# Optimization experiments

Measured on AMD Instinct MI355X. Metric: run time of the kernel, lower is better.

## Reference

```python
import jax, jax.numpy as jnp
import numpy as np

B, T, C = 2, 2048, 1024
N_HEAD = 16
G_NON = 32   # qgroup_size_non (layernorm / residual path)
G_LIN = 32   # qgroup_size_lin (linear path)
QMAX = 127.0
EPS = 1e-5


def quantize(x, G):
    """Group-wise symmetric int8 quantization along the last dim.
    Returns q (int8, same shape as x) and scales s with shape x.shape[:-1] + (D//G,)."""
    shp = x.shape
    xg = x.reshape(shp[:-1] + (shp[-1] // G, G))
    s = jnp.maximum(jnp.max(jnp.abs(xg), axis=-1) / QMAX, 1e-8)
    q = jnp.clip(jnp.round(xg / s[..., None]), -QMAX, QMAX).astype(jnp.int8)
    return q.reshape(shp), s


def dequant(q, s, G):
    shp = q.shape
    xg = q.astype(jnp.float32).reshape(shp[:-1] + (shp[-1] // G, G)) * s[..., None]
    return xg.reshape(shp)


def quant_dequant(x, G):
    """Fake-quantize (straight-through): forward = dequant(quantize(x))."""
    q, s = quantize(x, G)
    xd = dequant(q, s, G)
    return x + jax.lax.stop_gradient(xd - x)


def setup_inputs() -> dict:
    key = jax.random.key(0)
    k1, k2, k3, k4 = jax.random.split(key, 4)
    x = jax.random.normal(k1, (B, T, C), dtype=jnp.float32)
    # LN stats of x, produced by the previous block's int8_add_..._MeanVar
    mean = jnp.mean(x, axis=-1)
    rstd = 1.0 / jnp.sqrt(jnp.var(x, axis=-1) + EPS)
    qx, sx = quantize(x, G_NON)
    ln_w = 1.0 + 0.02 * jax.random.normal(k2, (C,), dtype=jnp.float32)
    w1 = 0.02 * jax.random.normal(k3, (3 * C, C), dtype=jnp.float32)   # c_attn.weight [out,in]
    w2 = 0.02 * jax.random.normal(k4, (C, C), dtype=jnp.float32)       # c_proj.weight [out,in]
    return {"x": x, "qx": qx.astype(jnp.int32), "sx": sx, "mean": mean,
            "rstd": rstd, "ln_w": ln_w, "w1": w1, "w2": w2}


def reference(x, qx, sx, mean, rstd, ln_w, w1, w2):
    hd = C // N_HEAD
    # ---- Part1: int8 layernorm (uses provided mean/rstd) + int8 c_attn linear ----
    ln_in = dequant(qx.astype(jnp.int8), sx, G_NON)               # [B,T,C]
    h = (ln_in - mean[..., None]) * rstd[..., None] * ln_w        # layernorm output
    hq = quant_dequant(h, G_NON)                                  # requantize activations
    w1q = quant_dequant(w1, G_LIN)                                # int8 weight
    qkv = jnp.einsum('btc,oc->bto', hq, w1q)                      # [B,T,3C]
    q, k, v = jnp.split(qkv, 3, axis=-1)
    q = q.reshape(B, T, N_HEAD, hd).transpose(0, 2, 1, 3)         # [B,H,T,hd]
    k = k.reshape(B, T, N_HEAD, hd).transpose(0, 2, 1, 3)
    v = v.reshape(B, T, N_HEAD, hd).transpose(0, 2, 1, 3)
    # ---- causal SDPA ----
    scores = jnp.einsum('bhqd,bhkd->bhqk', q, k) / jnp.sqrt(jnp.float32(hd))
    causal = jnp.tril(jnp.ones((T, T), dtype=bool))
    scores = jnp.where(causal, scores, jnp.float32(-1e30))
    attn = jax.nn.softmax(scores, axis=-1)
    y = jnp.einsum('bhqk,bhkd->bhqd', attn, v)
    y = y.transpose(0, 2, 1, 3).reshape(B, T, C)
    # ---- Part2: int8 c_proj linear + residual add with mean/var ----
    yq = quant_dequant(y, G_LIN)
    w2q = quant_dequant(w2, G_LIN)
    proj = jnp.einsum('btc,oc->bto', yq, w2q)
    fpx = x + proj                                                # fp residual output
    mean_o = jnp.mean(fpx, axis=-1)
    rstd_o = 1.0 / jnp.sqrt(jnp.var(fpx, axis=-1) + EPS)
    qo, so = quantize(fpx, G_NON)                                 # quantized output for next block
    return (fpx, qo, so, mean_o, rstd_o)
```

## Files before the change

### kernel.cpp

```cpp
#include <hip/hip_runtime.h>
#include <stdint.h>

#define BB 2
#define TT 2048
#define CC 1024
#define NH 16
#define HD 64
#define NG 32
#define ROWS (BB*TT)
#define C3 (3*CC)

typedef _Float16 half_t;
typedef __attribute__((ext_vector_type(8))) _Float16 half8;
typedef __attribute__((ext_vector_type(2))) __fp16 fp16x2;
typedef __attribute__((ext_vector_type(4))) float f32x4;

#define GLDS16(g, l) __builtin_amdgcn_global_load_lds( \
    (__attribute__((address_space(1))) void*)(g), \
    (__attribute__((address_space(3))) void*)(l), 16, 0, 0)

#define LOG2E 1.44269504f
#define DEFER_THR 5.5451774f

__device__ __forceinline__ uint32_t pk_h2(float a, float b) {
  union { fp16x2 h; uint32_t u; } cv;
  cv.h = __builtin_amdgcn_cvt_pkrtz(a, b);
  return cv.u;
}

__global__ void k_qdq_w(const float* __restrict__ w1, const float* __restrict__ w2,
                        half_t* __restrict__ o1, half_t* __restrict__ o2) {
  int g = blockIdx.x * blockDim.x + threadIdx.x;
  const float* src; half_t* dst; int gl;
  if (g < C3 * NG) { src = w1; dst = o1; gl = g; }
  else             { src = w2; dst = o2; gl = g - C3 * NG; }
  const float4* p = reinterpret_cast<const float4*>(src + (size_t)gl * 32);
  float v[32]; float amax = 0.f;
  #pragma unroll
  for (int i = 0; i < 8; ++i) {
    float4 t = p[i];
    v[4*i] = t.x; v[4*i+1] = t.y; v[4*i+2] = t.z; v[4*i+3] = t.w;
    amax = fmaxf(amax, fmaxf(fmaxf(fabsf(t.x), fabsf(t.y)), fmaxf(fabsf(t.z), fabsf(t.w))));
  }
  float s = fmaxf(amax / 127.0f, 1e-8f);
  half_t* o = dst + (size_t)gl * 32;
  #pragma unroll
  for (int c = 0; c < 4; ++c) {
    half8 ov;
    #pragma unroll
    for (int jj = 0; jj < 8; ++jj) {
      float q = fminf(fmaxf(rintf(v[c*8+jj] / s), -127.f), 127.f);
      ov[jj] = (half_t)(q * s);
    }
    *reinterpret_cast<half8*>(o + c*8) = ov;
  }
}

__global__ void k_qh(const int* __restrict__ qx, const float* __restrict__ sx,
                     const float* __restrict__ mean, const float* __restrict__ rstd,
                     const float* __restrict__ lnw, half_t* __restrict__ h16) {
  int g = blockIdx.x * blockDim.x + threadIdx.x;
  if (g >= ROWS * NG) return;
  int row = g >> 5, grp = g & 31;
  float sxv = sx[g];
  float mu = mean[row], rs = rstd[row];
  const int4* qp = reinterpret_cast<const int4*>(qx + (size_t)row * CC + grp * 32);
  const float4* wp = reinterpret_cast<const float4*>(lnw + grp * 32);
  float v[32]; float amax = 0.f;
  #pragma unroll
  for (int i = 0; i < 8; ++i) {
    int4 qv = qp[i]; float4 wv = wp[i];
    float h0 = ((float)qv.x * sxv - mu) * rs * wv.x;
    float h1 = ((float)qv.y * sxv - mu) * rs * wv.y;
    float h2 = ((float)qv.z * sxv - mu) * rs * wv.z;
    float h3 = ((float)qv.w * sxv - mu) * rs * wv.w;
    v[4*i] = h0; v[4*i+1] = h1; v[4*i+2] = h2; v[4*i+3] = h3;
    amax = fmaxf(amax, fmaxf(fmaxf(fabsf(h0), fabsf(h1)), fmaxf(fabsf(h2), fabsf(h3))));
  }
  float s = fmaxf(amax / 127.0f, 1e-8f);
  half_t* o = h16 + (size_t)row * CC + grp * 32;
  #pragma unroll
  for (int c = 0; c < 4; ++c) {
    half8 ov;
    #pragma unroll
    for (int jj = 0; jj < 8; ++jj) {
      float q = fminf(fmaxf(rintf(v[c*8+jj] / s), -127.f), 127.f);
      ov[jj] = (half_t)(q * s);
    }
    *reinterpret_cast<half8*>(o + c*8) = ov;
  }
}

template<typename TO>
__global__ __launch_bounds__(256) void k_gemm16(const half_t* __restrict__ A,
                                                const half_t* __restrict__ B,
                                                TO* __restrict__ Out, int N,
                                                int gx, int cpx, int klen) {
  __shared__ __align__(16) half_t As[2][128*32];
  __shared__ __align__(16) half_t Bs[2][128*32];
  const int tid = threadIdx.x;
  const int wave = tid >> 6, lane = tid & 63;
  const int l15 = lane & 15, lg = lane >> 4;
  const int flat = blockIdx.y * gx + blockIdx.x;
  const int swz = (flat & 7) * cpx + (flat >> 3);
  const int m0 = (swz / gx) * 128, n0 = (swz % gx) * 128;
  const int kbeg = blockIdx.z * klen;
  TO* out = Out + (size_t)blockIdx.z * ROWS * N;
  const int wm = (wave >> 1) * 64, wn = (wave & 1) * 64;
  f32x4 acc[4][4];
  #pragma unroll
  for (int i = 0; i < 4; ++i)
    #pragma unroll
    for (int jj = 0; jj < 4; ++jj) acc[i][jj] = f32x4{0.f, 0.f, 0.f, 0.f};
  const int srow = lane >> 2;
  const int scol = (lane & 3) * 8;
  const int seg0 = wave * 2;
  auto stage = [&](int buf, int k0) {
    #pragma unroll
    for (int s = 0; s < 2; ++s) {
      const int seg = seg0 + s;
      GLDS16(A + (size_t)(m0 + seg*16 + srow) * 1024 + k0 + scol, &As[buf][0] + seg*512);
      GLDS16(B + (size_t)(n0 + seg*16 + srow) * 1024 + k0 + scol, &Bs[buf][0] + seg*512);
    }
  };
  stage(0, kbeg);
  __syncthreads();
  int cur = 0;
  for (int k0 = kbeg; k0 < kbeg + klen; k0 += 32) {
    if (k0 + 32 < kbeg + klen) stage(cur ^ 1, k0 + 32);
    half8 af[4], bf[4];
    #pragma unroll
    for (int i = 0; i < 4; ++i) {
      af[i] = *reinterpret_cast<const half8*>(&As[cur][0] + (wm + i*16 + l15)*32 + lg*8);
      bf[i] = *reinterpret_cast<const half8*>(&Bs[cur][0] + (wn + i*16 + l15)*32 + lg*8);
    }
    #pragma unroll
    for (int mi = 0; mi < 4; ++mi)
      #pragma unroll
      for (int ni = 0; ni < 4; ++ni)
        acc[mi][ni] = __builtin_amdgcn_mfma_f32_16x16x32_f16(af[mi], bf[ni], acc[mi][ni], 0, 0, 0);
    __syncthreads();
    cur ^= 1;
  }
  const int crow = m0 + wm + lg * 4;
  const int ccol = n0 + wn + l15;
  #pragma unroll
  for (int mi = 0; mi < 4; ++mi)
    #pragma unroll
    for (int ni = 0; ni < 4; ++ni)
      #pragma unroll
      for (int r = 0; r < 4; ++r)
        out[(size_t)(crow + mi*16 + r) * N + ccol + ni*16] = (TO)acc[mi][ni][r];
}

__global__ __launch_bounds__(512, 4) void k_attn16(const half_t* __restrict__ qkv,
                                                   half_t* __restrict__ y16) {
  __shared__ __align__(16) half_t Ks[2][64*72];
  __shared__ __align__(16) half_t Vt[2][64*72];
  __shared__ __align__(16) half_t Ps[8][16*72];
  const int tid = threadIdx.x;
  const int wave = tid >> 6, lane = tid & 63;
  const int l15 = lane & 15, lg = lane >> 4;
  const int w4 = wave & 3;
  const int bh = blockIdx.x, b = bh >> 4, h = bh & 15;
  const int j = blockIdx.y;
  const int qtB = 31 - j;
  const int qt = (wave >> 2) ? qtB : j;

  const size_t row = (size_t)(b * TT + qt * 64 + w4 * 16 + l15);
  const half_t* qp = qkv + row * C3 + h * HD + lg * 8;
  const half8 q0 = *reinterpret_cast<const half8*>(qp)      * (half_t)0.125f;
  const half8 q1 = *reinterpret_cast<const half8*>(qp + 32) * (half_t)0.125f;

  float m = -3.0e38f;
  f32x4 yacc[4];
  f32x4 lacc = f32x4{0,0,0,0};
  #pragma unroll
  for (int n = 0; n < 4; ++n) yacc[n] = f32x4{0,0,0,0};

  const int sj = tid >> 3, sc = (tid & 7) * 8;
  const int vkp = tid >> 4, vd0 = (tid & 15) * 4;
  const int vxor = ((vd0 >> 3) & 7) << 2;
  const int pxor = (l15 & 3) << 3;
  half_t* pw = &Ps[wave][0];

  int vdw0[4], vdw1[4];
  #pragma unroll
  for (int n = 0; n < 4; ++n) {
    const int d = n*16 + l15;
    const int x = ((n*2 + (l15 >> 3)) & 7) << 2;
    vdw0[n] = (d*36 + lg*4) ^ x;
    vdw1[n] = (d*36 + 16 + lg*4) ^ x;
  }

  half8 ones8;
  #pragma unroll
  for (int i = 0; i < 8; ++i) ones8[i] = (half_t)1.0f;

  half8 k0r; uint2 u0r, u1r;
  const half_t* kvb = qkv + ((size_t)b * TT) * C3 + CC + h * HD;
  auto kload = [&](int kt) {
    const half_t* kp = kvb + (size_t)(kt*64 + sj) * C3 + sc;
    k0r = *reinterpret_cast<const half8*>(kp);
    const half_t* vp = kvb + (size_t)(kt*64 + vkp*2) * C3 + CC + vd0;
    u0r = *reinterpret_cast<const uint2*>(vp);
    u1r = *reinterpret_cast<const uint2*>(vp + C3);
  };
  auto stage = [&](int buf) {
    *reinterpret_cast<half8*>(&Ks[buf][0] + sj*72 + sc) = k0r;
    uint32_t* vt32 = reinterpret_cast<uint32_t*>(&Vt[buf][0]);
    vt32[((vd0+0)*36 + vkp) ^ vxor] = __builtin_amdgcn_perm(u1r.x, u0r.x, 0x05040100u);
    vt32[((vd0+1)*36 + vkp) ^ vxor] = __builtin_amdgcn_perm(u1r.x, u0r.x, 0x07060302u);
    vt32[((vd0+2)*36 + vkp) ^ vxor] = __builtin_amdgcn_perm(u1r.y, u0r.y, 0x05040100u);
    vt32[((vd0+3)*36 + vkp) ^ vxor] = __builtin_amdgcn_perm(u1r.y, u0r.y, 0x07060302u);
  };

  kload(0);
  stage(0);
  kload(1);
  __syncthreads();
  for (int kt = 0; kt <= qtB; ++kt) {
    const int cur = kt & 1;
    if (kt < qtB) {
      stage(cur ^ 1);
      if (kt + 2 <= qtB) kload(kt + 2);
    }
    if (kt <= qt) {
      const half_t* ksb = &Ks[cur][0];
      const uint32_t* vt32 = reinterpret_cast<const uint32_t*>(&Vt[cur][0]);
      f32x4 sacc[4];
      __builtin_amdgcn_s_setprio(1);
      #pragma unroll
      for (int kg = 0; kg < 4; ++kg) {
        const half8 a0 = *reinterpret_cast<const half8*>(ksb + (kg*16 + l15)*72 + lg*8);
        const half8 a1 = *reinterpret_cast<const half8*>(ksb + (kg*16 + l15)*72 + lg*8 + 32);
        f32x4 t = f32x4{0,0,0,0};
        t = __builtin_amdgcn_mfma_f32_16x16x32_f16(a0, q0, t, 0, 0, 0);
        t = __builtin_amdgcn_mfma_f32_16x16x32_f16(a1, q1, t, 0, 0, 0);
        sacc[kg] = t;
      }
      __builtin_amdgcn_s_setprio(0);
      float sv[16]; float tm = -3.0e38f;
      const bool diag = (kt == qt);
      #pragma unroll
      for (int kg = 0; kg < 4; ++kg)
        #pragma unroll
        for (int r = 0; r < 4; ++r) {
          float s = sacc[kg][r];
          if (diag && (kg*16 + lg*4 + r > w4*16 + l15)) s = -1e30f;
          sv[kg*4 + r] = s;
          tm = fmaxf(tm, s);
        }
      tm = fmaxf(tm, __shfl_xor(tm, 16));
      tm = fmaxf(tm, __shfl_xor(tm, 32));
      if (!__all(tm <= m + DEFER_THR)) {
        const float mn = fmaxf(m, tm);
        const float alpha = __builtin_amdgcn_exp2f((m - mn) * LOG2E);
        #pragma unroll
        for (int n = 0; n < 4; ++n) yacc[n] *= alpha;
        lacc *= alpha;
        m = mn;
      }
      const float nm = -m * LOG2E;
      #pragma unroll
      for (int i = 0; i < 16; ++i)
        sv[i] = __builtin_amdgcn_exp2f(fmaf(sv[i], LOG2E, nm));
      uint32_t* prow = reinterpret_cast<uint32_t*>(pw) + l15*36;
      #pragma unroll
      for (int kg = 0; kg < 4; ++kg) {
        uint2 pr;
        pr.x = pk_h2(sv[kg*4 + 0], sv[kg*4 + 1]);
        pr.y = pk_h2(sv[kg*4 + 2], sv[kg*4 + 3]);
        *reinterpret_cast<uint2*>(prow + ((kg*8 + lg*2) ^ pxor)) = pr;
      }
      __builtin_amdgcn_sched_barrier(0);
      const half8 pb0 = *reinterpret_cast<const half8*>(
          pw + (l15*36 + ((lg*4) ^ pxor)) * 2);
      const half8 pb1 = *reinterpret_cast<const half8*>(
          pw + (l15*36 + ((16 + lg*4) ^ pxor)) * 2);
      __builtin_amdgcn_s_setprio(1);
      #pragma unroll
      for (int n = 0; n < 4; ++n) {
        const half8 va0 = *reinterpret_cast<const half8*>(vt32 + vdw0[n]);
        const half8 va1 = *reinterpret_cast<const half8*>(vt32 + vdw1[n]);
        yacc[n] = __builtin_amdgcn_mfma_f32_16x16x32_f16(va0, pb0, yacc[n], 0, 0, 0);
        yacc[n] = __builtin_amdgcn_mfma_f32_16x16x32_f16(va1, pb1, yacc[n], 0, 0, 0);
      }
      lacc = __builtin_amdgcn_mfma_f32_16x16x32_f16(ones8, pb0, lacc, 0, 0, 0);
      lacc = __builtin_amdgcn_mfma_f32_16x16x32_f16(ones8, pb1, lacc, 0, 0, 0);
      __builtin_amdgcn_s_setprio(0);
    }
    __syncthreads();
  }

  const float inv = 1.0f / lacc[0];
  float v[16];
  #pragma unroll
  for (int n = 0; n < 4; ++n)
    #pragma unroll
    for (int r = 0; r < 4; ++r) v[n*4 + r] = yacc[n][r] * inv;
  half_t* yp = y16 + row * CC + h * HD;
  #pragma unroll
  for (int g = 0; g < 2; ++g) {
    float am = 0.f;
    #pragma unroll
    for (int t = 0; t < 8; ++t) am = fmaxf(am, fabsf(v[g*8 + t]));
    am = fmaxf(am, __shfl_xor(am, 16));
    am = fmaxf(am, __shfl_xor(am, 32));
    const float s = fmaxf(am / 127.0f, 1e-8f);
    const float qi = 1.0f / s;
    #pragma unroll
    for (int nn = 0; nn < 2; ++nn) {
      const int n = g*2 + nn;
      union { half_t h4[4]; uint64_t u; } pk;
      #pragma unroll
      for (int r = 0; r < 4; ++r) {
        float q = fminf(fmaxf(rintf(v[n*4 + r] * qi), -127.f), 127.f);
        pk.h4[r] = (half_t)(q * s);
      }
      *reinterpret_cast<uint64_t*>(yp + n*16 + lg*4) = pk.u;
    }
  }
}

__global__ __launch_bounds__(256) void k_final(
    const float* __restrict__ x, const half_t* __restrict__ p0,
    const half_t* __restrict__ p1,
    float* __restrict__ out_fpx, float* __restrict__ out_qo, float* __restrict__ out_so,
    float* __restrict__ out_mean, float* __restrict__ out_rstd) {
  __shared__ float red[16];
  int row = blockIdx.x;
  int tid = threadIdx.x;
  size_t base = (size_t)row * CC + tid * 4;
  float4 xv = *reinterpret_cast<const float4*>(x + base);
  union { uint64_t u; half_t h[4]; } pa, pb;
  pa.u = *reinterpret_cast<const uint64_t*>(p0 + base);
  pb.u = *reinterpret_cast<const uint64_t*>(p1 + base);
  float4 f;
  f.x = xv.x + (float)pa.h[0] + (float)pb.h[0];
  f.y = xv.y + (float)pa.h[1] + (float)pb.h[1];
  f.z = xv.z + (float)pa.h[2] + (float)pb.h[2];
  f.w = xv.w + (float)pa.h[3] + (float)pb.h[3];
  *reinterpret_cast<float4*>(out_fpx + base) = f;
  float sum = f.x + f.y + f.z + f.w;
  float sq  = f.x*f.x + f.y*f.y + f.z*f.z + f.w*f.w;
  #pragma unroll
  for (int off = 1; off < 64; off <<= 1) {
    sum += __shfl_xor(sum, off);
    sq  += __shfl_xor(sq, off);
  }
  int wid = tid >> 6, lane = tid & 63;
  if (lane == 0) { red[wid] = sum; red[8 + wid] = sq; }
  __syncthreads();
  if (tid == 0) {
    float s4 = red[0] + red[1] + red[2] + red[3];
    float q4 = red[8] + red[9] + red[10] + red[11];
    float mu = s4 * (1.0f / CC);
    float var = q4 * (1.0f / CC) - mu * mu;
    out_mean[row] = mu;
    out_rstd[row] = 1.0f / sqrtf(var + 1e-5f);
  }
  float amax = fmaxf(fmaxf(fabsf(f.x), fabsf(f.y)), fmaxf(fabsf(f.z), fabsf(f.w)));
  #pragma unroll
  for (int off = 1; off < 8; off <<= 1) amax = fmaxf(amax, __shfl_xor(amax, off, 8));
  float s = fmaxf(amax / 127.0f, 1e-8f);
  int g = tid >> 3, li = tid & 7;
  if (li == 0) out_so[row * NG + g] = s;
  float4 qo;
  qo.x = fminf(fmaxf(rintf(f.x / s), -127.f), 127.f);
  qo.y = fminf(fmaxf(rintf(f.y / s), -127.f), 127.f);
  qo.z = fminf(fmaxf(rintf(f.z / s), -127.f), 127.f);
  qo.w = fminf(fmaxf(rintf(f.w / s), -127.f), 127.f);
  *reinterpret_cast<float4*>(out_qo + base) = qo;
}

extern "C" void kernel_launch(void* const* d_in, const int* in_sizes, int n_in,
                              void* d_out, int out_size, void* d_ws, size_t ws_size,
                              hipStream_t stream) {
  const float* x    = (const float*)d_in[0];
  const int*   qx   = (const int*)d_in[1];
  const float* sx   = (const float*)d_in[2];
  const float* mean = (const float*)d_in[3];
  const float* rstd = (const float*)d_in[4];
  const float* lnw  = (const float*)d_in[5];
  const float* w1   = (const float*)d_in[6];
  const float* w2   = (const float*)d_in[7];

  float* out = (float*)d_out;
  float* o_fpx  = out;
  float* o_qo   = o_fpx + (size_t)ROWS * CC;
  float* o_so   = o_qo  + (size_t)ROWS * CC;
  float* o_mean = o_so  + (size_t)ROWS * NG;
  float* o_rstd = o_mean + ROWS;

  size_t off = 0;
  char* wsb = (char*)d_ws;
  auto alloc = [&](size_t bytes) -> void* {
    void* p = wsb + off;
    off += (bytes + 255) & ~(size_t)255;
    return p;
  };
  half_t* h16   = (half_t*)alloc((size_t)ROWS * CC * 2);
  half_t* w116  = (half_t*)alloc((size_t)C3 * CC * 2);
  half_t* w216  = (half_t*)alloc((size_t)CC * CC * 2);
  half_t* qkv16 = (half_t*)alloc((size_t)ROWS * C3 * 2);
  half_t* y16   = (half_t*)alloc((size_t)ROWS * CC * 2);
  half_t* proj  = (half_t*)alloc((size_t)2 * ROWS * CC * 2);

  k_qdq_w<<<(C3 * NG + CC * NG) / 256, 256, 0, stream>>>(w1, w2, w116, w216);
  k_qh<<<(ROWS * NG) / 256, 256, 0, stream>>>(qx, sx, mean, rstd, lnw, h16);
  k_gemm16<half_t><<<dim3(C3 / 128, ROWS / 128, 1), 256, 0, stream>>>(
      h16, w116, qkv16, C3, C3 / 128, (C3 / 128) * (ROWS / 128) / 8, 1024);
  k_attn16<<<dim3(BB * NH, 16), 512, 0, stream>>>(qkv16, y16);
  k_gemm16<half_t><<<dim3(CC / 128, ROWS / 128, 2), 256, 0, stream>>>(
      y16, w216, proj, CC, CC / 128, (CC / 128) * (ROWS / 128) / 8, 512);
  k_final<<<ROWS, 256, 0, stream>>>(x, proj, proj + (size_t)ROWS * CC,
                                    o_fpx, o_qo, o_so, o_mean, o_rstd);
}
```

Baseline: 125.9 us.

## Rewrite attention with 32x32 MFMA, register-resident P, and split-KV wave pairs

The attention kernel moves from 16x16x32 to 32x32x16 MFMA tiles. Each wave now owns 32 query rows, and the P tile stays in registers as the B operand, so the per-wave LDS round trip for P goes away. The row sum is taken directly instead of through a ones-vector MFMA. Wave pairs split the KV tiles by parity and merge their partial softmax states through shared memory at the end, with a permuted V column layout to match the new register mapping. The risks are higher register pressure from the 16-wide accumulators, an extra sync and merge step, and each wave doing work only every other KV tile.

```diff
diff --git a/kernel.cpp b/kernel.cpp
--- a/kernel.cpp
+++ b/kernel.cpp
@@ -14,6 +14,7 @@
 typedef __attribute__((ext_vector_type(8))) _Float16 half8;
 typedef __attribute__((ext_vector_type(2))) __fp16 fp16x2;
 typedef __attribute__((ext_vector_type(4))) float f32x4;
+typedef __attribute__((ext_vector_type(16))) float f32x16;
 
 #define GLDS16(g, l) __builtin_amdgcn_global_load_lds( \
     (__attribute__((address_space(1))) void*)(g), \
@@ -153,49 +154,41 @@
         out[(size_t)(crow + mi*16 + r) * N + ccol + ni*16] = (TO)acc[mi][ni][r];
 }
 
-__global__ __launch_bounds__(512, 4) void k_attn16(const half_t* __restrict__ qkv,
+__global__ __launch_bounds__(512, 4) void k_attn32(const half_t* __restrict__ qkv,
                                                    half_t* __restrict__ y16) {
-  __shared__ __align__(16) half_t Ks[2][64*72];
-  __shared__ __align__(16) half_t Vt[2][64*72];
-  __shared__ __align__(16) half_t Ps[8][16*72];
+  __shared__ __align__(16) half_t smem[4][64*72];
   const int tid = threadIdx.x;
   const int wave = tid >> 6, lane = tid & 63;
-  const int l15 = lane & 15, lg = lane >> 4;
-  const int w4 = wave & 3;
+  const int l31 = lane & 31, lh = lane >> 5;
   const int bh = blockIdx.x, b = bh >> 4, h = bh & 15;
   const int j = blockIdx.y;
-  const int qtB = 31 - j;
-  const int qt = (wave >> 2) ? qtB : j;
-
-  const size_t row = (size_t)(b * TT + qt * 64 + w4 * 16 + l15);
-  const half_t* qp = qkv + row * C3 + h * HD + lg * 8;
-  const half8 q0 = *reinterpret_cast<const half8*>(qp)      * (half_t)0.125f;
-  const half8 q1 = *reinterpret_cast<const half8*>(qp + 32) * (half_t)0.125f;
-
-  float m = -3.0e38f;
-  f32x4 yacc[4];
-  f32x4 lacc = f32x4{0,0,0,0};
-  #pragma unroll
-  for (int n = 0; n < 4; ++n) yacc[n] = f32x4{0,0,0,0};
+  const int tile = wave >> 2, par = (wave >> 1) & 1, rh = wave & 1;
+  const int qt = tile ? (31 - j) : j;
+  const int ktmax = 31 - j;
+
+  const size_t qrow = (size_t)(b * TT + qt * 64 + rh * 32 + l31);
+  const half_t* qp = qkv + qrow * C3 + h * HD + lh * 8;
+  half8 qreg[4];
+  #pragma unroll
+  for (int kk = 0; kk < 4; ++kk)
+    qreg[kk] = *reinterpret_cast<const half8*>(qp + kk * 16) * (half_t)0.125f;
+
+  float m = -3.0e38f, lsum = 0.f;
+  f32x16 yacc[2];
+  yacc[0] = (f32x16)(0.f); yacc[1] = (f32x16)(0.f);
 
   const int sj = tid >> 3, sc = (tid & 7) * 8;
   const int vkp = tid >> 4, vd0 = (tid & 15) * 4;
+  const int csp = (vkp & 0x19) | ((vkp & 2) << 1) | ((vkp & 4) >> 1);
   const int vxor = ((vd0 >> 3) & 7) << 2;
-  const int pxor = (l15 & 3) << 3;
-  half_t* pw = &Ps[wave][0];
-
-  int vdw0[4], vdw1[4];
-  #pragma unroll
-  for (int n = 0; n < 4; ++n) {
-    const int d = n*16 + l15;
-    const int x = ((n*2 + (l15 >> 3)) & 7) << 2;
-    vdw0[n] = (d*36 + lg*4) ^ x;
-    vdw1[n] = (d*36 + 16 + lg*4) ^ x;
-  }
-
-  half8 ones8;
-  #pragma unroll
-  for (int i = 0; i < 8; ++i) ones8[i] = (half_t)1.0f;
+
+  int vbase[2], vxr[2];
+  #pragma unroll
+  for (int db = 0; db < 2; ++db) {
+    const int d = db * 32 + l31;
+    vbase[db] = d * 36 + lh * 4;
+    vxr[db] = ((d >> 3) & 7) << 2;
+  }
 
   half8 k0r; uint2 u0r, u1r;
   const half_t* kvb = qkv + ((size_t)b * TT) * C3 + CC + h * HD;
@@ -207,118 +200,141 @@
     u1r = *reinterpret_cast<const uint2*>(vp + C3);
   };
   auto stage = [&](int buf) {
-    *reinterpret_cast<half8*>(&Ks[buf][0] + sj*72 + sc) = k0r;
-    uint32_t* vt32 = reinterpret_cast<uint32_t*>(&Vt[buf][0]);
-    vt32[((vd0+0)*36 + vkp) ^ vxor] = __builtin_amdgcn_perm(u1r.x, u0r.x, 0x05040100u);
-    vt32[((vd0+1)*36 + vkp) ^ vxor] = __builtin_amdgcn_perm(u1r.x, u0r.x, 0x07060302u);
-    vt32[((vd0+2)*36 + vkp) ^ vxor] = __builtin_amdgcn_perm(u1r.y, u0r.y, 0x05040100u);
-    vt32[((vd0+3)*36 + vkp) ^ vxor] = __builtin_amdgcn_perm(u1r.y, u0r.y, 0x07060302u);
+    *reinterpret_cast<half8*>(&smem[buf][0] + sj*72 + sc) = k0r;
+    uint32_t* vt32 = reinterpret_cast<uint32_t*>(&smem[2 + buf][0]);
+    vt32[(((vd0+0)*36 + csp)) ^ vxor] = __builtin_amdgcn_perm(u1r.x, u0r.x, 0x05040100u);
+    vt32[(((vd0+1)*36 + csp)) ^ vxor] = __builtin_amdgcn_perm(u1r.x, u0r.x, 0x07060302u);
+    vt32[(((vd0+2)*36 + csp)) ^ vxor] = __builtin_amdgcn_perm(u1r.y, u0r.y, 0x05040100u);
+    vt32[(((vd0+3)*36 + csp)) ^ vxor] = __builtin_amdgcn_perm(u1r.y, u0r.y, 0x07060302u);
   };
 
   kload(0);
   stage(0);
   kload(1);
   __syncthreads();
-  for (int kt = 0; kt <= qtB; ++kt) {
+  for (int kt = 0; kt <= ktmax; ++kt) {
     const int cur = kt & 1;
-    if (kt < qtB) {
+    if (kt < ktmax) {
       stage(cur ^ 1);
-      if (kt + 2 <= qtB) kload(kt + 2);
-    }
-    if (kt <= qt) {
-      const half_t* ksb = &Ks[cur][0];
-      const uint32_t* vt32 = reinterpret_cast<const uint32_t*>(&Vt[cur][0]);
-      f32x4 sacc[4];
+      if (kt + 2 <= ktmax) kload(kt + 2);
+    }
+    if (((kt & 1) == par) && kt <= qt) {
+      const half_t* ksb = &smem[cur][0];
+      const uint32_t* vt32 = reinterpret_cast<const uint32_t*>(&smem[2 + cur][0]);
+      f32x16 sacc[2];
+      sacc[0] = (f32x16)(0.f); sacc[1] = (f32x16)(0.f);
       __builtin_amdgcn_s_setprio(1);
       #pragma unroll
-      for (int kg = 0; kg < 4; ++kg) {
-        const half8 a0 = *reinterpret_cast<const half8*>(ksb + (kg*16 + l15)*72 + lg*8);
-        const half8 a1 = *reinterpret_cast<const half8*>(ksb + (kg*16 + l15)*72 + lg*8 + 32);
-        f32x4 t = f32x4{0,0,0,0};
-        t = __builtin_amdgcn_mfma_f32_16x16x32_f16(a0, q0, t, 0, 0, 0);
-        t = __builtin_amdgcn_mfma_f32_16x16x32_f16(a1, q1, t, 0, 0, 0);
-        sacc[kg] = t;
-      }
+      for (int kb = 0; kb < 2; ++kb)
+        #pragma unroll
+        for (int kk = 0; kk < 4; ++kk) {
+          const half8 a = *reinterpret_cast<const half8*>(
+              ksb + (kb*32 + l31)*72 + kk*16 + lh*8);
+          sacc[kb] = __builtin_amdgcn_mfma_f32_32x32x16_f16(a, qreg[kk], sacc[kb], 0, 0, 0);
+        }
       __builtin_amdgcn_s_setprio(0);
-      float sv[16]; float tm = -3.0e38f;
+      float sv[2][16]; float tm = -3.0e38f;
       const bool diag = (kt == qt);
-      #pragma unroll
-      for (int kg = 0; kg < 4; ++kg)
-        #pragma unroll
-        for (int r = 0; r < 4; ++r) {
-          float s = sacc[kg][r];
-          if (diag && (kg*16 + lg*4 + r > w4*16 + l15)) s = -1e30f;
-          sv[kg*4 + r] = s;
+      const int qloc = rh * 32 + l31;
+      #pragma unroll
+      for (int kb = 0; kb < 2; ++kb)
+        #pragma unroll
+        for (int r = 0; r < 16; ++r) {
+          float s = sacc[kb][r];
+          if (diag && (kb*32 + (r&3) + 8*(r>>2) + 4*lh > qloc)) s = -1e30f;
+          sv[kb][r] = s;
           tm = fmaxf(tm, s);
         }
-      tm = fmaxf(tm, __shfl_xor(tm, 16));
       tm = fmaxf(tm, __shfl_xor(tm, 32));
       if (!__all(tm <= m + DEFER_THR)) {
         const float mn = fmaxf(m, tm);
         const float alpha = __builtin_amdgcn_exp2f((m - mn) * LOG2E);
-        #pragma unroll
-        for (int n = 0; n < 4; ++n) yacc[n] *= alpha;
-        lacc *= alpha;
+        yacc[0] *= alpha; yacc[1] *= alpha;
+        lsum *= alpha;
         m = mn;
       }
       const float nm = -m * LOG2E;
-      #pragma unroll
-      for (int i = 0; i < 16; ++i)
-        sv[i] = __builtin_amdgcn_exp2f(fmaf(sv[i], LOG2E, nm));
-      uint32_t* prow = reinterpret_cast<uint32_t*>(pw) + l15*36;
-      #pragma unroll
-      for (int kg = 0; kg < 4; ++kg) {
-        uint2 pr;
-        pr.x = pk_h2(sv[kg*4 + 0], sv[kg*4 + 1]);
-        pr.y = pk_h2(sv[kg*4 + 2], sv[kg*4 + 3]);
-        *reinterpret_cast<uint2*>(prow + ((kg*8 + lg*2) ^ pxor)) = pr;
+      float rs = 0.f;
+      #pragma unroll
+      for (int kb = 0; kb < 2; ++kb)
+        #pragma unroll
+        for (int r = 0; r < 16; ++r) {
+          sv[kb][r] = __builtin_amdgcn_exp2f(fmaf(sv[kb][r], LOG2E, nm));
+          rs += sv[kb][r];
+        }
+      lsum += rs;
+      uint32_t w[2][8];
+      #pragma unroll
+      for (int kb = 0; kb < 2; ++kb)
+        #pragma unroll
+        for (int r2 = 0; r2 < 8; ++r2)
+          w[kb][r2] = pk_h2(sv[kb][2*r2], sv[kb][2*r2+1]);
+      __builtin_amdgcn_s_setprio(1);
+      #pragma unroll
+      for (int db = 0; db < 2; ++db)
+        #pragma unroll
+        for (int kb = 0; kb < 2; ++kb)
+          #pragma unroll
+          for (int kk = 0; kk < 2; ++kk) {
+            const int gdw = (vbase[db] + kb*16 + kk*8) ^ vxr[db];
+            const half8 va = *reinterpret_cast<const half8*>(vt32 + gdw);
+            union { uint32_t u[4]; half8 h; } bf;
+            bf.u[0] = w[kb][4*kk + 0]; bf.u[1] = w[kb][4*kk + 1];
+            bf.u[2] = w[kb][4*kk + 2]; bf.u[3] = w[kb][4*kk + 3];
+            yacc[db] = __builtin_amdgcn_mfma_f32_32x32x16_f16(va, bf.h, yacc[db], 0, 0, 0);
+          }
+      __builtin_amdgcn_s_setprio(0);
+    }
+    __syncthreads();
+  }
+
+  float* mb = reinterpret_cast<float*>(&smem[0][0]);
+  const int pr = tile * 2 + rh;
+  float* yb = mb + pr * 2176;
+  if (par == 0) {
+    #pragma unroll
+    for (int db = 0; db < 2; ++db)
+      #pragma unroll
+      for (int r = 0; r < 16; ++r)
+        yb[(db*16 + r) * 64 + lane] = yacc[db][r];
+    yb[2048 + lane] = m;
+    yb[2112 + lane] = lsum;
+  }
+  __syncthreads();
+  if (par == 1) {
+    const float me = yb[2048 + lane];
+    const float le = yb[2112 + lane];
+    const float M = fmaxf(m, me);
+    const float ae = __builtin_amdgcn_exp2f((me - M) * LOG2E);
+    const float ao = __builtin_amdgcn_exp2f((m - M) * LOG2E);
+    float lt = le * ae + lsum * ao;
+    lt += __shfl_xor(lt, 32);
+    const float inv = 1.0f / lt;
+    float yv[2][16];
+    #pragma unroll
+    for (int db = 0; db < 2; ++db)
+      #pragma unroll
+      for (int r = 0; r < 16; ++r)
+        yv[db][r] = (yb[(db*16 + r) * 64 + lane] * ae + yacc[db][r] * ao) * inv;
+    half_t* yp = y16 + qrow * CC + h * HD;
+    #pragma unroll
+    for (int db = 0; db < 2; ++db) {
+      float am = 0.f;
+      #pragma unroll
+      for (int r = 0; r < 16; ++r) am = fmaxf(am, fabsf(yv[db][r]));
+      am = fmaxf(am, __shfl_xor(am, 32));
+      const float s = fmaxf(am / 127.0f, 1e-8f);
+      const float qi = 1.0f / s;
+      #pragma unroll
+      for (int t = 0; t < 4; ++t) {
+        union { half_t h4[4]; uint64_t u; } pk;
+        #pragma unroll
+        for (int rr = 0; rr < 4; ++rr) {
+          float q = fminf(fmaxf(rintf(yv[db][4*t + rr] * qi), -127.f), 127.f);
+          pk.h4[rr] = (half_t)(q * s);
+        }
+        *reinterpret_cast<uint64_t*>(yp + db*32 + 8*t + 4*lh) = pk.u;
       }
-      __builtin_amdgcn_sched_barrier(0);
-      const half8 pb0 = *reinterpret_cast<const half8*>(
-          pw + (l15*36 + ((lg*4) ^ pxor)) * 2);
-      const half8 pb1 = *reinterpret_cast<const half8*>(
-          pw + (l15*36 + ((16 + lg*4) ^ pxor)) * 2);
-      __builtin_amdgcn_s_setprio(1);
-      #pragma unroll
-      for (int n = 0; n < 4; ++n) {
-        const half8 va0 = *reinterpret_cast<const half8*>(vt32 + vdw0[n]);
-        const half8 va1 = *reinterpret_cast<const half8*>(vt32 + vdw1[n]);
-        yacc[n] = __builtin_amdgcn_mfma_f32_16x16x32_f16(va0, pb0, yacc[n], 0, 0, 0);
-        yacc[n] = __builtin_amdgcn_mfma_f32_16x16x32_f16(va1, pb1, yacc[n], 0, 0, 0);
-      }
-      lacc = __builtin_amdgcn_mfma_f32_16x16x32_f16(ones8, pb0, lacc, 0, 0, 0);
-      lacc = __builtin_amdgcn_mfma_f32_16x16x32_f16(ones8, pb1, lacc, 0, 0, 0);
-      __builtin_amdgcn_s_setprio(0);
-    }
-    __syncthreads();
-  }
-
-  const float inv = 1.0f / lacc[0];
-  float v[16];
-  #pragma unroll
-  for (int n = 0; n < 4; ++n)
-    #pragma unroll
-    for (int r = 0; r < 4; ++r) v[n*4 + r] = yacc[n][r] * inv;
-  half_t* yp = y16 + row * CC + h * HD;
-  #pragma unroll
-  for (int g = 0; g < 2; ++g) {
-    float am = 0.f;
-    #pragma unroll
-    for (int t = 0; t < 8; ++t) am = fmaxf(am, fabsf(v[g*8 + t]));
-    am = fmaxf(am, __shfl_xor(am, 16));
-    am = fmaxf(am, __shfl_xor(am, 32));
-    const float s = fmaxf(am / 127.0f, 1e-8f);
-    const float qi = 1.0f / s;
-    #pragma unroll
-    for (int nn = 0; nn < 2; ++nn) {
-      const int n = g*2 + nn;
-      union { half_t h4[4]; uint64_t u; } pk;
-      #pragma unroll
-      for (int r = 0; r < 4; ++r) {
-        float q = fminf(fmaxf(rintf(v[n*4 + r] * qi), -127.f), 127.f);
-        pk.h4[r] = (half_t)(q * s);
-      }
-      *reinterpret_cast<uint64_t*>(yp + n*16 + lg*4) = pk.u;
     }
   }
 }
@@ -411,7 +427,7 @@
   k_qh<<<(ROWS * NG) / 256, 256, 0, stream>>>(qx, sx, mean, rstd, lnw, h16);
   k_gemm16<half_t><<<dim3(C3 / 128, ROWS / 128, 1), 256, 0, stream>>>(
       h16, w116, qkv16, C3, C3 / 128, (C3 / 128) * (ROWS / 128) / 8, 1024);
-  k_attn16<<<dim3(BB * NH, 16), 512, 0, stream>>>(qkv16, y16);
+  k_attn32<<<dim3(BB * NH, 16), 512, 0, stream>>>(qkv16, y16);
   k_gemm16<half_t><<<dim3(CC / 128, ROWS / 128, 2), 256, 0, stream>>>(
       y16, w216, proj, CC, CC / 128, (CC / 128) * (ROWS / 128) / 8, 512);
   k_final<<<ROWS, 256, 0, stream>>>(x, proj, proj + (size_t)ROWS * CC,
```

Result: slower. 141.1 us (+12.0%).
